# Performance work log

Measured on AMD Instinct MI355X. Metric: run time of the kernel, lower is better.

Reference implementation:

```python
import jax, jax.numpy as jnp
from jax import lax
import numpy as np

SLOPE = 0.1  # LeakyReLU negative slope used throughout DA_conv


def setup_inputs() -> dict:
    key = jax.random.key(0)
    ks = jax.random.split(key, 8)
    B, C, H, W = 16, 64, 160, 160
    Cout, red = 64, 8
    feat = jax.random.normal(ks[0], (B, C, H, W), dtype=jnp.float32)
    deg = jax.random.normal(ks[1], (B, C, 1, 1), dtype=jnp.float32)
    W1 = jax.random.normal(ks[2], (64, C), dtype=jnp.float32) * 0.05
    W2 = jax.random.normal(ks[3], (Cout * 9, 64), dtype=jnp.float32) * 0.05
    Wc = jax.random.normal(ks[4], (Cout, Cout), dtype=jnp.float32) * 0.05
    bc = jnp.zeros((Cout,), dtype=jnp.float32)
    Wd1 = jax.random.normal(ks[5], (red, C), dtype=jnp.float32) * 0.05
    Wd2 = jax.random.normal(ks[6], (Cout, red), dtype=jnp.float32) * 0.05
    return {"feat": feat, "deg": deg, "W1": W1, "W2": W2, "Wc": Wc,
            "bc": bc, "Wd1": Wd1, "Wd2": Wd2}


def reference(feat, deg, W1, W2, Wc, bc, Wd1, Wd2):
    B, C, H, W = feat.shape
    Cout = Wc.shape[0]
    KS = 3
    d = deg[:, :, 0, 0]  # [B, C]

    # --- dynamic per-sample, per-channel 3x3 kernel generation ---
    h = jax.nn.leaky_relu(d @ W1.T, SLOPE)            # [B, 64]
    k = (h @ W2.T).reshape(B * Cout, 1, KS, KS)        # [B*Cout, 1, 3, 3]

    # grouped depthwise conv: input [1, B*C, H, W], groups = B*C
    x = feat.reshape(1, B * C, H, W)
    out = lax.conv_general_dilated(
        x, k, window_strides=(1, 1), padding=[(1, 1), (1, 1)],
        dimension_numbers=("NCHW", "OIHW", "NCHW"),
        feature_group_count=B * C)
    out = jax.nn.leaky_relu(out, SLOPE).reshape(B, Cout, H, W)

    # 1x1 conv with bias (common.default_conv)
    out = jnp.einsum("oi,bihw->bohw", Wc, out) + bc[None, :, None, None]

    # --- channel attention branch (1x1 convs == matmuls on [B,C]) ---
    a = jax.nn.leaky_relu(jnp.einsum("ri,bi->br", Wd1, d), SLOPE)   # [B, red]
    att = jax.nn.sigmoid(jnp.einsum("or,br->bo", Wd2, a))           # [B, Cout]

    return out + feat * att[:, :, None, None]
```

## Files before the change

kernel.cpp:

```cpp
#include <hip/hip_runtime.h>
#include <hip/hip_bf16.h>
#include <math.h>

#define SLOPE 0.1f
#define B_ 16
#define C_ 64
#define H_ 160
#define W_ 160
#define HW_ (H_*W_)

typedef short bf16x8 __attribute__((ext_vector_type(8)));
typedef float f32x4  __attribute__((ext_vector_type(4)));
typedef unsigned int uint2v __attribute__((ext_vector_type(2)));

__device__ __forceinline__ float lrelu(float x) { return fmaxf(x, SLOPE * x); }
__device__ __forceinline__ unsigned f2bf(float x) {
  union { float f; unsigned u; } c; c.f = x;
  return (c.u + 0x7fffu + ((c.u >> 16) & 1u)) >> 16;
}
__device__ __forceinline__ float bf2f(unsigned short u) {
  union { unsigned u; float f; } c; c.u = ((unsigned)u) << 16; return c.f;
}

__device__ __forceinline__ void gl2lds16(const void* g, void* l) {
  __builtin_amdgcn_global_load_lds(
      (const __attribute__((address_space(1))) void*)g,
      (__attribute__((address_space(3))) void*)l, 16, 0, 0);
}

__global__ __launch_bounds__(64) void prep_kernel(
    const float* __restrict__ deg,
    const float* __restrict__ W1,
    const float* __restrict__ W2,
    const float* __restrict__ Wd1,
    const float* __restrict__ Wd2,
    float* __restrict__ ws) {
  const int b = blockIdx.x;
  const int j = threadIdx.x;
  __shared__ float sd[64], sh[64], sa[8];
  sd[j] = deg[b * 64 + j];
  __syncthreads();

  float acc = 0.f;
  for (int i = 0; i < 64; ++i) acc = fmaf(sd[i], W1[j * 64 + i], acc);
  sh[j] = lrelu(acc);

  if (j < 8) {
    float s = 0.f;
    for (int i = 0; i < 64; ++i) s = fmaf(sd[i], Wd1[j * 64 + i], s);
    sa[j] = lrelu(s);
  }
  __syncthreads();

  float kv[9];
#pragma unroll
  for (int t = 0; t < 9; ++t) kv[t] = 0.f;
  for (int l = 0; l < 64; ++l) {
    float hl = sh[l];
#pragma unroll
    for (int t = 0; t < 9; ++t) kv[t] = fmaf(hl, W2[(j * 9 + t) * 64 + l], kv[t]);
  }
  const int slot = ((j & 15) >> 2) * 16 + (j >> 4) * 4 + (j & 3);
  unsigned short* kw = (unsigned short*)(ws + 1024) + (b * 64 + slot) * 16;
#pragma unroll
  for (int t = 0; t < 9; ++t) kw[t] = (unsigned short)f2bf(kv[t]);
#pragma unroll
  for (int t = 9; t < 16; ++t) kw[t] = 0;

  float s2 = 0.f;
#pragma unroll
  for (int r = 0; r < 8; ++r) s2 = fmaf(Wd2[j * 8 + r], sa[r], s2);
  ws[b * 64 + j] = 1.f / (1.f + __expf(-s2));
}

__global__ __launch_bounds__(256, 4) void main_kernel(
    const float* __restrict__ feat,
    const float* __restrict__ Wc,
    const float* __restrict__ bc,
    const float* __restrict__ ws,
    float* __restrict__ out) {
  __shared__ __align__(16) float S[2][16][240];
  __shared__ __align__(16) unsigned short Tt[2048];
  __shared__ __align__(16) unsigned short Ff[2048];
  __shared__ __align__(16) unsigned short Kl[1024];

  const int rb  = blockIdx.x;
  const int bid = (rb & 7) * 400 + (rb >> 3);
  const int b   = bid / 200;
  const int rem = bid - b * 200;
  const int ty  = rem / 10, tx = rem - ty * 10;
  const int x0 = tx * 16, y0 = ty * 8;
  const int tid = threadIdx.x;
  const int lane = tid & 63, wid = tid >> 6;

  const float* __restrict__ attp  = ws + b * 64;
  const char*  __restrict__ kb8   = (const char*)(ws + 1024) + b * 2048;
  const float* __restrict__ plane = feat + (size_t)(b * 64) * HW_;

  const int ci = tid >> 4;
  const int q  = (tid >> 2) & 3;
  const int h  = tid & 3;
  const int nl = lane & 15, kg = lane >> 4;
  const int ochunk = wid * 16;

  const int srow = lane / 6;
  const int schk = lane - srow * 6;
  const int grow = min(max(y0 + srow - 1, 0), H_ - 1);
  const int gcol = min(max(x0 - 4 + schk * 4, 0), W_ - 4);
  const float* sp0 = plane + grow * W_ + gcol;

  union AF { bf16x8 v; unsigned short u[8]; };
  AF a[4];
  const unsigned short ab = (unsigned short)f2bf(attp[ochunk + nl]);
#pragma unroll
  for (int g = 0; g < 4; ++g) {
    const float4 w = *(const float4*)(Wc + (ochunk + nl) * 64 + g * 16 + 4 * kg);
    a[g].u[0] = (unsigned short)f2bf(w.x); a[g].u[1] = (unsigned short)f2bf(w.y);
    a[g].u[2] = (unsigned short)f2bf(w.z); a[g].u[3] = (unsigned short)f2bf(w.w);
#pragma unroll
    for (int j = 0; j < 4; ++j)
      a[g].u[4 + j] = (wid == g && nl == 4 * kg + j) ? ab : (unsigned short)0;
  }
  const float4 bcv = *(const float4*)(bc + ochunk + 4 * kg);

  asm volatile("s_waitcnt vmcnt(0)" ::: "memory");

  if (lane < 32) gl2lds16(kb8 + wid * 512 + lane * 16, &Kl[wid * 256]);
#define STAGE(g_, bf_) \
  if (lane < 60) { \
    const float* s_ = sp0 + (size_t)((g_) * 16 + wid * 4) * HW_; \
    gl2lds16(s_,            &S[bf_][wid * 4 + 0][0]); \
    gl2lds16(s_ + HW_,      &S[bf_][wid * 4 + 1][0]); \
    gl2lds16(s_ + 2 * HW_,  &S[bf_][wid * 4 + 2][0]); \
    gl2lds16(s_ + 3 * HW_,  &S[bf_][wid * 4 + 3][0]); \
  }
  STAGE(0, 0);
  STAGE(1, 1);

  f32x4 acc[8];
#pragma unroll
  for (int nt = 0; nt < 8; ++nt) acc[nt] = (f32x4){0.f, 0.f, 0.f, 0.f};

  const float mlz = (x0 == 0 && q == 0) ? 0.f : 1.f;
  const float mrz = (x0 == W_ - 16 && q == 3) ? 0.f : 1.f;

  const unsigned t_base = (unsigned)(uintptr_t)&Tt[0] + (unsigned)(lane * 8);
  const unsigned f_base = (unsigned)(uintptr_t)&Ff[0] + (unsigned)(lane * 8);
  union BU { bf16x8 v; uint2v qv[2]; };

#pragma unroll
  for (int g = 0; g < 4; ++g) {
    const int sb = g & 1;
    if (g < 3) {
      asm volatile("s_waitcnt vmcnt(4)" ::: "memory");
    } else {
      asm volatile("s_waitcnt vmcnt(0)" ::: "memory");
    }
    __builtin_amdgcn_sched_barrier(0);

    const unsigned short* kr = &Kl[(wid * 16 + g * 4 + (lane >> 4)) * 16];
    union KU { uint4 v; unsigned short u[8]; } k07;
    k07.v = *(const uint4*)kr;
    const unsigned short k8u = kr[8];
    float kk[9];
#pragma unroll
    for (int t = 0; t < 8; ++t) kk[t] = bf2f(k07.u[t]);
    kk[8] = bf2f(k8u);

    float rv[4][9];
#pragma unroll
    for (int rr = 0; rr < 4; ++rr) {
      const float* sp = &S[sb][ci][(2 * h + rr) * 24 + 4 * q];
      const f32x4 v0 = *(const f32x4*)sp;
      const f32x4 v1 = *(const f32x4*)(sp + 4);
      rv[rr][0] = v0[0]; rv[rr][1] = v0[1]; rv[rr][2] = v0[2];
      rv[rr][3] = v0[3] * mlz;
      rv[rr][4] = v1[0]; rv[rr][5] = v1[1]; rv[rr][6] = v1[2]; rv[rr][7] = v1[3];
      rv[rr][8] = sp[8] * mrz;
    }

#pragma unroll
    for (int rr = 0; rr < 2; ++rr) {
      const int srw = 2 * h + rr;
      const float mt = (srw == 0 && y0 == 0) ? 0.f : 1.f;
      const float mb = (srw == 7 && y0 == H_ - 8) ? 0.f : 1.f;
      float sv[4], fv[4];
#pragma unroll
      for (int j = 0; j < 4; ++j) {
        float ts = fmaf(rv[rr][j + 5], kk[2], fmaf(rv[rr][j + 4], kk[1], rv[rr][j + 3] * kk[0]));
        float cs = fmaf(rv[rr + 1][j + 5], kk[5], fmaf(rv[rr + 1][j + 4], kk[4], rv[rr + 1][j + 3] * kk[3]));
        float bs = fmaf(rv[rr + 2][j + 5], kk[8], fmaf(rv[rr + 2][j + 4], kk[7], rv[rr + 2][j + 3] * kk[6]));
        sv[j] = fmaf(mt, ts, fmaf(mb, bs, cs));
        fv[j] = rv[rr + 1][j + 4];
      }
      uint2v tq, fq;
      tq.x = f2bf(lrelu(sv[0])) | (f2bf(lrelu(sv[1])) << 16);
      tq.y = f2bf(lrelu(sv[2])) | (f2bf(lrelu(sv[3])) << 16);
      fq.x = f2bf(fv[0]) | (f2bf(fv[1]) << 16);
      fq.y = f2bf(fv[2]) | (f2bf(fv[3]) << 16);
      const int tidx = srw * 256 + ci * 16 + 4 * q;
      *(uint2v*)&Tt[tidx] = tq;
      *(uint2v*)&Ff[tidx] = fq;
    }

    if (g < 2) { STAGE(g + 2, sb); }

    asm volatile("s_waitcnt lgkmcnt(0)" ::: "memory");
    __builtin_amdgcn_sched_barrier(0);
    __builtin_amdgcn_s_barrier();
    __builtin_amdgcn_sched_barrier(0);

    if (wid == g) {
      uint2v t0, t1, t2, t3, t4, t5, t6, t7;
      uint2v f0, f1, f2, f3, f4, f5, f6, f7;
      asm volatile("ds_read_b64_tr_b16 %0, %1 offset:0"    : "=v"(t0) : "v"(t_base));
      asm volatile("ds_read_b64_tr_b16 %0, %1 offset:512"  : "=v"(t1) : "v"(t_base));
      asm volatile("ds_read_b64_tr_b16 %0, %1 offset:0"    : "=v"(f0) : "v"(f_base));
      asm volatile("ds_read_b64_tr_b16 %0, %1 offset:512"  : "=v"(f1) : "v"(f_base));
      asm volatile("ds_read_b64_tr_b16 %0, %1 offset:1024" : "=v"(t2) : "v"(t_base));
      asm volatile("ds_read_b64_tr_b16 %0, %1 offset:1536" : "=v"(t3) : "v"(t_base));
      asm volatile("ds_read_b64_tr_b16 %0, %1 offset:1024" : "=v"(f2) : "v"(f_base));
      asm volatile("ds_read_b64_tr_b16 %0, %1 offset:1536" : "=v"(f3) : "v"(f_base));
      asm volatile("s_waitcnt lgkmcnt(4)" ::: "memory");
      __builtin_amdgcn_sched_barrier(0);
      {
        BU u0, u1;
        u0.qv[0] = t0; u0.qv[1] = f0;
        u1.qv[0] = t1; u1.qv[1] = f1;
        acc[0] = __builtin_amdgcn_mfma_f32_16x16x32_bf16(a[g].v, u0.v, acc[0], 0, 0, 0);
        acc[1] = __builtin_amdgcn_mfma_f32_16x16x32_bf16(a[g].v, u1.v, acc[1], 0, 0, 0);
      }
      asm volatile("ds_read_b64_tr_b16 %0, %1 offset:2048" : "=v"(t4) : "v"(t_base));
      asm volatile("ds_read_b64_tr_b16 %0, %1 offset:2560" : "=v"(t5) : "v"(t_base));
      asm volatile("ds_read_b64_tr_b16 %0, %1 offset:2048" : "=v"(f4) : "v"(f_base));
      asm volatile("ds_read_b64_tr_b16 %0, %1 offset:2560" : "=v"(f5) : "v"(f_base));
      asm volatile("s_waitcnt lgkmcnt(4)" ::: "memory");
      __builtin_amdgcn_sched_barrier(0);
      {
        BU u2, u3;
        u2.qv[0] = t2; u2.qv[1] = f2;
        u3.qv[0] = t3; u3.qv[1] = f3;
        acc[2] = __builtin_amdgcn_mfma_f32_16x16x32_bf16(a[g].v, u2.v, acc[2], 0, 0, 0);
        acc[3] = __builtin_amdgcn_mfma_f32_16x16x32_bf16(a[g].v, u3.v, acc[3], 0, 0, 0);
      }
      asm volatile("ds_read_b64_tr_b16 %0, %1 offset:3072" : "=v"(t6) : "v"(t_base));
      asm volatile("ds_read_b64_tr_b16 %0, %1 offset:3584" : "=v"(t7) : "v"(t_base));
      asm volatile("ds_read_b64_tr_b16 %0, %1 offset:3072" : "=v"(f6) : "v"(f_base));
      asm volatile("ds_read_b64_tr_b16 %0, %1 offset:3584" : "=v"(f7) : "v"(f_base));
      asm volatile("s_waitcnt lgkmcnt(4)" ::: "memory");
      __builtin_amdgcn_sched_barrier(0);
      {
        BU u4, u5;
        u4.qv[0] = t4; u4.qv[1] = f4;
        u5.qv[0] = t5; u5.qv[1] = f5;
        acc[4] = __builtin_amdgcn_mfma_f32_16x16x32_bf16(a[g].v, u4.v, acc[4], 0, 0, 0);
        acc[5] = __builtin_amdgcn_mfma_f32_16x16x32_bf16(a[g].v, u5.v, acc[5], 0, 0, 0);
      }
      asm volatile("s_waitcnt lgkmcnt(0)" ::: "memory");
      __builtin_amdgcn_sched_barrier(0);
      {
        BU u6, u7;
        u6.qv[0] = t6; u6.qv[1] = f6;
        u7.qv[0] = t7; u7.qv[1] = f7;
        acc[6] = __builtin_amdgcn_mfma_f32_16x16x32_bf16(a[g].v, u6.v, acc[6], 0, 0, 0);
        acc[7] = __builtin_amdgcn_mfma_f32_16x16x32_bf16(a[g].v, u7.v, acc[7], 0, 0, 0);
      }
    } else {
      uint2v ta0, ta1, ta2, ta3, tb0, tb1, tb2, tb3;
      asm volatile("ds_read_b64_tr_b16 %0, %1 offset:0"    : "=v"(ta0) : "v"(t_base));
      asm volatile("ds_read_b64_tr_b16 %0, %1 offset:512"  : "=v"(ta1) : "v"(t_base));
      asm volatile("ds_read_b64_tr_b16 %0, %1 offset:1024" : "=v"(ta2) : "v"(t_base));
      asm volatile("ds_read_b64_tr_b16 %0, %1 offset:1536" : "=v"(ta3) : "v"(t_base));
      asm volatile("s_waitcnt lgkmcnt(0)" ::: "memory");
      __builtin_amdgcn_sched_barrier(0);
      asm volatile("ds_read_b64_tr_b16 %0, %1 offset:2048" : "=v"(tb0) : "v"(t_base));
      asm volatile("ds_read_b64_tr_b16 %0, %1 offset:2560" : "=v"(tb1) : "v"(t_base));
      asm volatile("ds_read_b64_tr_b16 %0, %1 offset:3072" : "=v"(tb2) : "v"(t_base));
      asm volatile("ds_read_b64_tr_b16 %0, %1 offset:3584" : "=v"(tb3) : "v"(t_base));
      {
        BU u0, u1, u2, u3;
        u0.qv[0] = ta0; u0.qv[1] = (uint2v){0u, 0u};
        u1.qv[0] = ta1; u1.qv[1] = (uint2v){0u, 0u};
        u2.qv[0] = ta2; u2.qv[1] = (uint2v){0u, 0u};
        u3.qv[0] = ta3; u3.qv[1] = (uint2v){0u, 0u};
        acc[0] = __builtin_amdgcn_mfma_f32_16x16x32_bf16(a[g].v, u0.v, acc[0], 0, 0, 0);
        acc[1] = __builtin_amdgcn_mfma_f32_16x16x32_bf16(a[g].v, u1.v, acc[1], 0, 0, 0);
        acc[2] = __builtin_amdgcn_mfma_f32_16x16x32_bf16(a[g].v, u2.v, acc[2], 0, 0, 0);
        acc[3] = __builtin_amdgcn_mfma_f32_16x16x32_bf16(a[g].v, u3.v, acc[3], 0, 0, 0);
      }
      asm volatile("s_waitcnt lgkmcnt(0)" ::: "memory");
      __builtin_amdgcn_sched_barrier(0);
      {
        BU u4, u5, u6, u7;
        u4.qv[0] = tb0; u4.qv[1] = (uint2v){0u, 0u};
        u5.qv[0] = tb1; u5.qv[1] = (uint2v){0u, 0u};
        u6.qv[0] = tb2; u6.qv[1] = (uint2v){0u, 0u};
        u7.qv[0] = tb3; u7.qv[1] = (uint2v){0u, 0u};
        acc[4] = __builtin_amdgcn_mfma_f32_16x16x32_bf16(a[g].v, u4.v, acc[4], 0, 0, 0);
        acc[5] = __builtin_amdgcn_mfma_f32_16x16x32_bf16(a[g].v, u5.v, acc[5], 0, 0, 0);
        acc[6] = __builtin_amdgcn_mfma_f32_16x16x32_bf16(a[g].v, u6.v, acc[6], 0, 0, 0);
        acc[7] = __builtin_amdgcn_mfma_f32_16x16x32_bf16(a[g].v, u7.v, acc[7], 0, 0, 0);
      }
    }
    __builtin_amdgcn_s_barrier();
    __builtin_amdgcn_sched_barrier(0);
  }
#undef STAGE

  const int ob = ochunk + 4 * kg;
  float* __restrict__ outb = out + (size_t)(b * 64) * HW_;
#pragma unroll
  for (int nt = 0; nt < 8; ++nt) {
    const int off = (y0 + nt) * W_ + x0 + nl;
    outb[(size_t)(ob + 0) * HW_ + off] = acc[nt][0] + bcv.x;
    outb[(size_t)(ob + 1) * HW_ + off] = acc[nt][1] + bcv.y;
    outb[(size_t)(ob + 2) * HW_ + off] = acc[nt][2] + bcv.z;
    outb[(size_t)(ob + 3) * HW_ + off] = acc[nt][3] + bcv.w;
  }
}

extern "C" void kernel_launch(void* const* d_in, const int* in_sizes, int n_in,
                              void* d_out, int out_size, void* d_ws, size_t ws_size,
                              hipStream_t stream) {
  const float* feat = (const float*)d_in[0];
  const float* deg  = (const float*)d_in[1];
  const float* W1   = (const float*)d_in[2];
  const float* W2   = (const float*)d_in[3];
  const float* Wc   = (const float*)d_in[4];
  const float* bc   = (const float*)d_in[5];
  const float* Wd1  = (const float*)d_in[6];
  const float* Wd2  = (const float*)d_in[7];
  float* out = (float*)d_out;
  float* ws  = (float*)d_ws;

  prep_kernel<<<dim3(B_), dim3(64), 0, stream>>>(deg, W1, W2, Wd1, Wd2, ws);
  main_kernel<<<dim3(3200), dim3(256), 0, stream>>>(feat, Wc, bc, ws, out);
}
```

Before: 67.17 us.

## Convert main kernel to persistent blocks with atomic tile scheduler

The main kernel launches 1024 persistent blocks that grab 8x16 tiles from a global atomic counter, which prep_kernel resets, instead of launching one block per tile. Per-block setup such as the bf16 Wc fragments and bias is hoisted out of the tile loop. The per-sample kernel weights are packed at 12 halves per channel instead of 16, and the attention diagonal fragment is rebuilt per tile. The aim is to cut block launch and setup overhead and balance load, at the cost of an atomic and a __syncthreads per tile and no cross-tile overlap of loads.

```diff
diff --git a/kernel.cpp b/kernel.cpp
--- a/kernel.cpp
+++ b/kernel.cpp
@@ -8,6 +8,8 @@
 #define H_ 160
 #define W_ 160
 #define HW_ (H_*W_)
+#define NTILES 3200
+#define WS_CTR_OFF 28672
 
 typedef short bf16x8 __attribute__((ext_vector_type(8)));
 typedef float f32x4  __attribute__((ext_vector_type(4)));
@@ -61,71 +63,59 @@
     for (int t = 0; t < 9; ++t) kv[t] = fmaf(hl, W2[(j * 9 + t) * 64 + l], kv[t]);
   }
   const int slot = ((j & 15) >> 2) * 16 + (j >> 4) * 4 + (j & 3);
-  unsigned short* kw = (unsigned short*)(ws + 1024) + (b * 64 + slot) * 16;
+  unsigned short* kw = (unsigned short*)((char*)ws + 4096) + (b * 64 + slot) * 12;
 #pragma unroll
   for (int t = 0; t < 9; ++t) kw[t] = (unsigned short)f2bf(kv[t]);
-#pragma unroll
-  for (int t = 9; t < 16; ++t) kw[t] = 0;
+  kw[9] = 0; kw[10] = 0; kw[11] = 0;
 
   float s2 = 0.f;
 #pragma unroll
   for (int r = 0; r < 8; ++r) s2 = fmaf(Wd2[j * 8 + r], sa[r], s2);
   ws[b * 64 + j] = 1.f / (1.f + __expf(-s2));
+
+  if (b == 0 && j == 0) *(unsigned*)((char*)ws + WS_CTR_OFF) = 0u;
 }
 
 __global__ __launch_bounds__(256, 4) void main_kernel(
     const float* __restrict__ feat,
     const float* __restrict__ Wc,
     const float* __restrict__ bc,
-    const float* __restrict__ ws,
+    float* __restrict__ ws,
     float* __restrict__ out) {
   __shared__ __align__(16) float S[2][16][240];
   __shared__ __align__(16) unsigned short Tt[2048];
   __shared__ __align__(16) unsigned short Ff[2048];
-  __shared__ __align__(16) unsigned short Kl[1024];
-
-  const int rb  = blockIdx.x;
-  const int bid = (rb & 7) * 400 + (rb >> 3);
-  const int b   = bid / 200;
-  const int rem = bid - b * 200;
-  const int ty  = rem / 10, tx = rem - ty * 10;
-  const int x0 = tx * 16, y0 = ty * 8;
+  __shared__ __align__(16) unsigned short Kl[768];
+  __shared__ int sTile;
+
   const int tid = threadIdx.x;
   const int lane = tid & 63, wid = tid >> 6;
-
-  const float* __restrict__ attp  = ws + b * 64;
-  const char*  __restrict__ kb8   = (const char*)(ws + 1024) + b * 2048;
-  const float* __restrict__ plane = feat + (size_t)(b * 64) * HW_;
-
   const int ci = tid >> 4;
   const int q  = (tid >> 2) & 3;
   const int h  = tid & 3;
   const int nl = lane & 15, kg = lane >> 4;
   const int ochunk = wid * 16;
-
   const int srow = lane / 6;
   const int schk = lane - srow * 6;
-  const int grow = min(max(y0 + srow - 1, 0), H_ - 1);
-  const int gcol = min(max(x0 - 4 + schk * 4, 0), W_ - 4);
-  const float* sp0 = plane + grow * W_ + gcol;
+
+  unsigned* ctr = (unsigned*)((char*)ws + WS_CTR_OFF);
 
   union AF { bf16x8 v; unsigned short u[8]; };
   AF a[4];
-  const unsigned short ab = (unsigned short)f2bf(attp[ochunk + nl]);
 #pragma unroll
   for (int g = 0; g < 4; ++g) {
     const float4 w = *(const float4*)(Wc + (ochunk + nl) * 64 + g * 16 + 4 * kg);
     a[g].u[0] = (unsigned short)f2bf(w.x); a[g].u[1] = (unsigned short)f2bf(w.y);
     a[g].u[2] = (unsigned short)f2bf(w.z); a[g].u[3] = (unsigned short)f2bf(w.w);
-#pragma unroll
-    for (int j = 0; j < 4; ++j)
-      a[g].u[4 + j] = (wid == g && nl == 4 * kg + j) ? ab : (unsigned short)0;
+    a[g].u[4] = 0; a[g].u[5] = 0; a[g].u[6] = 0; a[g].u[7] = 0;
   }
   const float4 bcv = *(const float4*)(bc + ochunk + 4 * kg);
-
   asm volatile("s_waitcnt vmcnt(0)" ::: "memory");
 
-  if (lane < 32) gl2lds16(kb8 + wid * 512 + lane * 16, &Kl[wid * 256]);
+  const unsigned t_base = (unsigned)(uintptr_t)&Tt[0] + (unsigned)(lane * 8);
+  const unsigned f_base = (unsigned)(uintptr_t)&Ff[0] + (unsigned)(lane * 8);
+  union BU { bf16x8 v; uint2v qv[2]; };
+
 #define STAGE(g_, bf_) \
   if (lane < 60) { \
     const float* s_ = sp0 + (size_t)((g_) * 16 + wid * 4) * HW_; \
@@ -134,189 +124,215 @@
     gl2lds16(s_ + 2 * HW_,  &S[bf_][wid * 4 + 2][0]); \
     gl2lds16(s_ + 3 * HW_,  &S[bf_][wid * 4 + 3][0]); \
   }
-  STAGE(0, 0);
-  STAGE(1, 1);
-
-  f32x4 acc[8];
-#pragma unroll
-  for (int nt = 0; nt < 8; ++nt) acc[nt] = (f32x4){0.f, 0.f, 0.f, 0.f};
-
-  const float mlz = (x0 == 0 && q == 0) ? 0.f : 1.f;
-  const float mrz = (x0 == W_ - 16 && q == 3) ? 0.f : 1.f;
-
-  const unsigned t_base = (unsigned)(uintptr_t)&Tt[0] + (unsigned)(lane * 8);
-  const unsigned f_base = (unsigned)(uintptr_t)&Ff[0] + (unsigned)(lane * 8);
-  union BU { bf16x8 v; uint2v qv[2]; };
-
-#pragma unroll
-  for (int g = 0; g < 4; ++g) {
-    const int sb = g & 1;
-    if (g < 3) {
-      asm volatile("s_waitcnt vmcnt(4)" ::: "memory");
-    } else {
-      asm volatile("s_waitcnt vmcnt(0)" ::: "memory");
-    }
-    __builtin_amdgcn_sched_barrier(0);
-
-    const unsigned short* kr = &Kl[(wid * 16 + g * 4 + (lane >> 4)) * 16];
-    union KU { uint4 v; unsigned short u[8]; } k07;
-    k07.v = *(const uint4*)kr;
-    const unsigned short k8u = kr[8];
-    float kk[9];
-#pragma unroll
-    for (int t = 0; t < 8; ++t) kk[t] = bf2f(k07.u[t]);
-    kk[8] = bf2f(k8u);
-
-    float rv[4][9];
-#pragma unroll
-    for (int rr = 0; rr < 4; ++rr) {
-      const float* sp = &S[sb][ci][(2 * h + rr) * 24 + 4 * q];
-      const f32x4 v0 = *(const f32x4*)sp;
-      const f32x4 v1 = *(const f32x4*)(sp + 4);
-      rv[rr][0] = v0[0]; rv[rr][1] = v0[1]; rv[rr][2] = v0[2];
-      rv[rr][3] = v0[3] * mlz;
-      rv[rr][4] = v1[0]; rv[rr][5] = v1[1]; rv[rr][6] = v1[2]; rv[rr][7] = v1[3];
-      rv[rr][8] = sp[8] * mrz;
-    }
-
-#pragma unroll
-    for (int rr = 0; rr < 2; ++rr) {
-      const int srw = 2 * h + rr;
-      const float mt = (srw == 0 && y0 == 0) ? 0.f : 1.f;
-      const float mb = (srw == 7 && y0 == H_ - 8) ? 0.f : 1.f;
-      float sv[4], fv[4];
-#pragma unroll
-      for (int j = 0; j < 4; ++j) {
-        float ts = fmaf(rv[rr][j + 5], kk[2], fmaf(rv[rr][j + 4], kk[1], rv[rr][j + 3] * kk[0]));
-        float cs = fmaf(rv[rr + 1][j + 5], kk[5], fmaf(rv[rr + 1][j + 4], kk[4], rv[rr + 1][j + 3] * kk[3]));
-        float bs = fmaf(rv[rr + 2][j + 5], kk[8], fmaf(rv[rr + 2][j + 4], kk[7], rv[rr + 2][j + 3] * kk[6]));
-        sv[j] = fmaf(mt, ts, fmaf(mb, bs, cs));
-        fv[j] = rv[rr + 1][j + 4];
+
+  for (;;) {
+    if (tid == 0) sTile = (int)atomicAdd(ctr, 1u);
+    __syncthreads();
+    const int tl = sTile;
+    if (tl >= NTILES) break;
+
+    const int b   = tl / 200;
+    const int rem = tl - b * 200;
+    const int ty  = rem / 10, tx = rem - ty * 10;
+    const int x0 = tx * 16, y0 = ty * 8;
+
+    const float* __restrict__ plane = feat + (size_t)(b * 64) * HW_;
+    const char*  __restrict__ kb8   = (const char*)ws + 4096 + b * 1536;
+    const float abf = ws[b * 64 + ochunk + nl];
+
+    const int grow = min(max(y0 + srow - 1, 0), H_ - 1);
+    const int gcol = min(max(x0 - 4 + schk * 4, 0), W_ - 4);
+    const float* sp0 = plane + grow * W_ + gcol;
+    const float mlz = (x0 == 0 && q == 0) ? 0.f : 1.f;
+    const float mrz = (x0 == W_ - 16 && q == 3) ? 0.f : 1.f;
+
+    if (lane < 24) gl2lds16(kb8 + wid * 384 + lane * 16, &Kl[wid * 192]);
+    STAGE(0, 0);
+    STAGE(1, 1);
+
+    f32x4 acc[8];
+#pragma unroll
+    for (int nt = 0; nt < 8; ++nt) acc[nt] = (f32x4){0.f, 0.f, 0.f, 0.f};
+
+#pragma unroll
+    for (int g = 0; g < 4; ++g) {
+      const int sb = g & 1;
+      if (g < 3) {
+        asm volatile("s_waitcnt vmcnt(4)" ::: "memory");
+      } else {
+        asm volatile("s_waitcnt vmcnt(0)" ::: "memory");
       }
-      uint2v tq, fq;
-      tq.x = f2bf(lrelu(sv[0])) | (f2bf(lrelu(sv[1])) << 16);
-      tq.y = f2bf(lrelu(sv[2])) | (f2bf(lrelu(sv[3])) << 16);
-      fq.x = f2bf(fv[0]) | (f2bf(fv[1]) << 16);
-      fq.y = f2bf(fv[2]) | (f2bf(fv[3]) << 16);
-      const int tidx = srw * 256 + ci * 16 + 4 * q;
-      *(uint2v*)&Tt[tidx] = tq;
-      *(uint2v*)&Ff[tidx] = fq;
-    }
-
-    if (g < 2) { STAGE(g + 2, sb); }
-
-    asm volatile("s_waitcnt lgkmcnt(0)" ::: "memory");
-    __builtin_amdgcn_sched_barrier(0);
-    __builtin_amdgcn_s_barrier();
-    __builtin_amdgcn_sched_barrier(0);
-
-    if (wid == g) {
-      uint2v t0, t1, t2, t3, t4, t5, t6, t7;
-      uint2v f0, f1, f2, f3, f4, f5, f6, f7;
-      asm volatile("ds_read_b64_tr_b16 %0, %1 offset:0"    : "=v"(t0) : "v"(t_base));
-      asm volatile("ds_read_b64_tr_b16 %0, %1 offset:512"  : "=v"(t1) : "v"(t_base));
-      asm volatile("ds_read_b64_tr_b16 %0, %1 offset:0"    : "=v"(f0) : "v"(f_base));
-      asm volatile("ds_read_b64_tr_b16 %0, %1 offset:512"  : "=v"(f1) : "v"(f_base));
-      asm volatile("ds_read_b64_tr_b16 %0, %1 offset:1024" : "=v"(t2) : "v"(t_base));
-      asm volatile("ds_read_b64_tr_b16 %0, %1 offset:1536" : "=v"(t3) : "v"(t_base));
-      asm volatile("ds_read_b64_tr_b16 %0, %1 offset:1024" : "=v"(f2) : "v"(f_base));
-      asm volatile("ds_read_b64_tr_b16 %0, %1 offset:1536" : "=v"(f3) : "v"(f_base));
-      asm volatile("s_waitcnt lgkmcnt(4)" ::: "memory");
       __builtin_amdgcn_sched_barrier(0);
-      {
-        BU u0, u1;
-        u0.qv[0] = t0; u0.qv[1] = f0;
-        u1.qv[0] = t1; u1.qv[1] = f1;
-        acc[0] = __builtin_amdgcn_mfma_f32_16x16x32_bf16(a[g].v, u0.v, acc[0], 0, 0, 0);
-        acc[1] = __builtin_amdgcn_mfma_f32_16x16x32_bf16(a[g].v, u1.v, acc[1], 0, 0, 0);
+
+      const unsigned short* kr = &Kl[(wid * 16 + g * 4 + (lane >> 4)) * 12];
+      union KU { uint2v v; unsigned short u[4]; };
+      KU kA, kB;
+      kA.v = *(const uint2v*)(kr);
+      kB.v = *(const uint2v*)(kr + 4);
+      const unsigned short k8u = kr[8];
+      float kk[9];
+#pragma unroll
+      for (int t = 0; t < 4; ++t) { kk[t] = bf2f(kA.u[t]); kk[4 + t] = bf2f(kB.u[t]); }
+      kk[8] = bf2f(k8u);
+
+      float rv[4][9];
+#pragma unroll
+      for (int rr = 0; rr < 4; ++rr) {
+        const float* sp = &S[sb][ci][(2 * h + rr) * 24 + 4 * q];
+        const f32x4 v0 = *(const f32x4*)sp;
+        const f32x4 v1 = *(const f32x4*)(sp + 4);
+        rv[rr][0] = v0[0]; rv[rr][1] = v0[1]; rv[rr][2] = v0[2];
+        rv[rr][3] = v0[3] * mlz;
+        rv[rr][4] = v1[0]; rv[rr][5] = v1[1]; rv[rr][6] = v1[2]; rv[rr][7] = v1[3];
+        rv[rr][8] = sp[8] * mrz;
       }
-      asm volatile("ds_read_b64_tr_b16 %0, %1 offset:2048" : "=v"(t4) : "v"(t_base));
-      asm volatile("ds_read_b64_tr_b16 %0, %1 offset:2560" : "=v"(t5) : "v"(t_base));
-      asm volatile("ds_read_b64_tr_b16 %0, %1 offset:2048" : "=v"(f4) : "v"(f_base));
-      asm volatile("ds_read_b64_tr_b16 %0, %1 offset:2560" : "=v"(f5) : "v"(f_base));
-      asm volatile("s_waitcnt lgkmcnt(4)" ::: "memory");
-      __builtin_amdgcn_sched_barrier(0);
-      {
-        BU u2, u3;
-        u2.qv[0] = t2; u2.qv[1] = f2;
-        u3.qv[0] = t3; u3.qv[1] = f3;
-        acc[2] = __builtin_amdgcn_mfma_f32_16x16x32_bf16(a[g].v, u2.v, acc[2], 0, 0, 0);
-        acc[3] = __builtin_amdgcn_mfma_f32_16x16x32_bf16(a[g].v, u3.v, acc[3], 0, 0, 0);
+
+#pragma unroll
+      for (int rr = 0; rr < 2; ++rr) {
+        const int srw = 2 * h + rr;
+        const float mt = (srw == 0 && y0 == 0) ? 0.f : 1.f;
+        const float mb = (srw == 7 && y0 == H_ - 8) ? 0.f : 1.f;
+        float sv[4], fv[4];
+#pragma unroll
+        for (int j = 0; j < 4; ++j) {
+          float ts = fmaf(rv[rr][j + 5], kk[2], fmaf(rv[rr][j + 4], kk[1], rv[rr][j + 3] * kk[0]));
+          float cs = fmaf(rv[rr + 1][j + 5], kk[5], fmaf(rv[rr + 1][j + 4], kk[4], rv[rr + 1][j + 3] * kk[3]));
+          float bs = fmaf(rv[rr + 2][j + 5], kk[8], fmaf(rv[rr + 2][j + 4], kk[7], rv[rr + 2][j + 3] * kk[6]));
+          sv[j] = fmaf(mt, ts, fmaf(mb, bs, cs));
+          fv[j] = rv[rr + 1][j + 4];
+        }
+        uint2v tq, fq;
+        tq.x = f2bf(lrelu(sv[0])) | (f2bf(lrelu(sv[1])) << 16);
+        tq.y = f2bf(lrelu(sv[2])) | (f2bf(lrelu(sv[3])) << 16);
+        fq.x = f2bf(fv[0]) | (f2bf(fv[1]) << 16);
+        fq.y = f2bf(fv[2]) | (f2bf(fv[3]) << 16);
+        const int tidx = srw * 256 + ci * 16 + 4 * q;
+        *(uint2v*)&Tt[tidx] = tq;
+        *(uint2v*)&Ff[tidx] = fq;
       }
-      asm volatile("ds_read_b64_tr_b16 %0, %1 offset:3072" : "=v"(t6) : "v"(t_base));
-      asm volatile("ds_read_b64_tr_b16 %0, %1 offset:3584" : "=v"(t7) : "v"(t_base));
-      asm volatile("ds_read_b64_tr_b16 %0, %1 offset:3072" : "=v"(f6) : "v"(f_base));
-      asm volatile("ds_read_b64_tr_b16 %0, %1 offset:3584" : "=v"(f7) : "v"(f_base));
-      asm volatile("s_waitcnt lgkmcnt(4)" ::: "memory");
-      __builtin_amdgcn_sched_barrier(0);
-      {
-        BU u4, u5;
-        u4.qv[0] = t4; u4.qv[1] = f4;
-        u5.qv[0] = t5; u5.qv[1] = f5;
-        acc[4] = __builtin_amdgcn_mfma_f32_16x16x32_bf16(a[g].v, u4.v, acc[4], 0, 0, 0);
-        acc[5] = __builtin_amdgcn_mfma_f32_16x16x32_bf16(a[g].v, u5.v, acc[5], 0, 0, 0);
-      }
+
+      if (g < 2) { STAGE(g + 2, sb); }
+
       asm volatile("s_waitcnt lgkmcnt(0)" ::: "memory");
       __builtin_amdgcn_sched_barrier(0);
-      {
-        BU u6, u7;
-        u6.qv[0] = t6; u6.qv[1] = f6;
-        u7.qv[0] = t7; u7.qv[1] = f7;
-        acc[6] = __builtin_amdgcn_mfma_f32_16x16x32_bf16(a[g].v, u6.v, acc[6], 0, 0, 0);
-        acc[7] = __builtin_amdgcn_mfma_f32_16x16x32_bf16(a[g].v, u7.v, acc[7], 0, 0, 0);
+      __builtin_amdgcn_s_barrier();
+      __builtin_amdgcn_sched_barrier(0);
+
+      if (wid == g) {
+        AF adiag;
+        adiag.v = a[g].v;
+        const unsigned short abu = (unsigned short)f2bf(abf);
+#pragma unroll
+        for (int j = 0; j < 4; ++j)
+          adiag.u[4 + j] = (nl == 4 * kg + j) ? abu : (unsigned short)0;
+
+        uint2v t0, t1, t2, t3, t4, t5, t6, t7;
+        uint2v f0, f1, f2, f3, f4, f5, f6, f7;
+        asm volatile("ds_read_b64_tr_b16 %0, %1 offset:0"    : "=v"(t0) : "v"(t_base));
+        asm volatile("ds_read_b64_tr_b16 %0, %1 offset:512"  : "=v"(t1) : "v"(t_base));
+        asm volatile("ds_read_b64_tr_b16 %0, %1 offset:0"    : "=v"(f0) : "v"(f_base));
+        asm volatile("ds_read_b64_tr_b16 %0, %1 offset:512"  : "=v"(f1) : "v"(f_base));
+        asm volatile("ds_read_b64_tr_b16 %0, %1 offset:1024" : "=v"(t2) : "v"(t_base));
+        asm volatile("ds_read_b64_tr_b16 %0, %1 offset:1536" : "=v"(t3) : "v"(t_base));
+        asm volatile("ds_read_b64_tr_b16 %0, %1 offset:1024" : "=v"(f2) : "v"(f_base));
+        asm volatile("ds_read_b64_tr_b16 %0, %1 offset:1536" : "=v"(f3) : "v"(f_base));
+        asm volatile("s_waitcnt lgkmcnt(4)" ::: "memory");
+        __builtin_amdgcn_sched_barrier(0);
+        {
+          BU u0, u1;
+          u0.qv[0] = t0; u0.qv[1] = f0;
+          u1.qv[0] = t1; u1.qv[1] = f1;
+          acc[0] = __builtin_amdgcn_mfma_f32_16x16x32_bf16(adiag.v, u0.v, acc[0], 0, 0, 0);
+          acc[1] = __builtin_amdgcn_mfma_f32_16x16x32_bf16(adiag.v, u1.v, acc[1], 0, 0, 0);
+        }
+        asm volatile("ds_read_b64_tr_b16 %0, %1 offset:2048" : "=v"(t4) : "v"(t_base));
+        asm volatile("ds_read_b64_tr_b16 %0, %1 offset:2560" : "=v"(t5) : "v"(t_base));
+        asm volatile("ds_read_b64_tr_b16 %0, %1 offset:2048" : "=v"(f4) : "v"(f_base));
+        asm volatile("ds_read_b64_tr_b16 %0, %1 offset:2560" : "=v"(f5) : "v"(f_base));
+        asm volatile("s_waitcnt lgkmcnt(4)" ::: "memory");
+        __builtin_amdgcn_sched_barrier(0);
+        {
+          BU u2, u3;
+          u2.qv[0] = t2; u2.qv[1] = f2;
+          u3.qv[0] = t3; u3.qv[1] = f3;
+          acc[2] = __builtin_amdgcn_mfma_f32_16x16x32_bf16(adiag.v, u2.v, acc[2], 0, 0, 0);
+          acc[3] = __builtin_amdgcn_mfma_f32_16x16x32_bf16(adiag.v, u3.v, acc[3], 0, 0, 0);
+        }
+        asm volatile("ds_read_b64_tr_b16 %0, %1 offset:3072" : "=v"(t6) : "v"(t_base));
+        asm volatile("ds_read_b64_tr_b16 %0, %1 offset:3584" : "=v"(t7) : "v"(t_base));
+        asm volatile("ds_read_b64_tr_b16 %0, %1 offset:3072" : "=v"(f6) : "v"(f_base));
+        asm volatile("ds_read_b64_tr_b16 %0, %1 offset:3584" : "=v"(f7) : "v"(f_base));
+        asm volatile("s_waitcnt lgkmcnt(4)" ::: "memory");
+        __builtin_amdgcn_sched_barrier(0);
+        {
+          BU u4, u5;
+          u4.qv[0] = t4; u4.qv[1] = f4;
+          u5.qv[0] = t5; u5.qv[1] = f5;
+          acc[4] = __builtin_amdgcn_mfma_f32_16x16x32_bf16(adiag.v, u4.v, acc[4], 0, 0, 0);
+          acc[5] = __builtin_amdgcn_mfma_f32_16x16x32_bf16(adiag.v, u5.v, acc[5], 0, 0, 0);
+        }
+        asm volatile("s_waitcnt lgkmcnt(0)" ::: "memory");
+        __builtin_amdgcn_sched_barrier(0);
+        {
+          BU u6, u7;
+          u6.qv[0] = t6; u6.qv[1] = f6;
+          u7.qv[0] = t7; u7.qv[1] = f7;
+          acc[6] = __builtin_amdgcn_mfma_f32_16x16x32_bf16(adiag.v, u6.v, acc[6], 0, 0, 0);
+          acc[7] = __builtin_amdgcn_mfma_f32_16x16x32_bf16(adiag.v, u7.v, acc[7], 0, 0, 0);
+        }
+      } else {
+        uint2v ta0, ta1, ta2, ta3, tb0, tb1, tb2, tb3;
+        asm volatile("ds_read_b64_tr_b16 %0, %1 offset:0"    : "=v"(ta0) : "v"(t_base));
+        asm volatile("ds_read_b64_tr_b16 %0, %1 offset:512"  : "=v"(ta1) : "v"(t_base));
+        asm volatile("ds_read_b64_tr_b16 %0, %1 offset:1024" : "=v"(ta2) : "v"(t_base));
+        asm volatile("ds_read_b64_tr_b16 %0, %1 offset:1536" : "=v"(ta3) : "v"(t_base));
+        asm volatile("s_waitcnt lgkmcnt(0)" ::: "memory");
+        __builtin_amdgcn_sched_barrier(0);
+        asm volatile("ds_read_b64_tr_b16 %0, %1 offset:2048" : "=v"(tb0) : "v"(t_base));
+        asm volatile("ds_read_b64_tr_b16 %0, %1 offset:2560" : "=v"(tb1) : "v"(t_base));
+        asm volatile("ds_read_b64_tr_b16 %0, %1 offset:3072" : "=v"(tb2) : "v"(t_base));
+        asm volatile("ds_read_b64_tr_b16 %0, %1 offset:3584" : "=v"(tb3) : "v"(t_base));
+        {
+          BU u0, u1, u2, u3;
+          u0.qv[0] = ta0; u0.qv[1] = (uint2v){0u, 0u};
+          u1.qv[0] = ta1; u1.qv[1] = (uint2v){0u, 0u};
+          u2.qv[0] = ta2; u2.qv[1] = (uint2v){0u, 0u};
+          u3.qv[0] = ta3; u3.qv[1] = (uint2v){0u, 0u};
+          acc[0] = __builtin_amdgcn_mfma_f32_16x16x32_bf16(a[g].v, u0.v, acc[0], 0, 0, 0);
+          acc[1] = __builtin_amdgcn_mfma_f32_16x16x32_bf16(a[g].v, u1.v, acc[1], 0, 0, 0);
+          acc[2] = __builtin_amdgcn_mfma_f32_16x16x32_bf16(a[g].v, u2.v, acc[2], 0, 0, 0);
+          acc[3] = __builtin_amdgcn_mfma_f32_16x16x32_bf16(a[g].v, u3.v, acc[3], 0, 0, 0);
+        }
+        asm volatile("s_waitcnt lgkmcnt(0)" ::: "memory");
+        __builtin_amdgcn_sched_barrier(0);
+        {
+          BU u4, u5, u6, u7;
+          u4.qv[0] = tb0; u4.qv[1] = (uint2v){0u, 0u};
+          u5.qv[0] = tb1; u5.qv[1] = (uint2v){0u, 0u};
+          u6.qv[0] = tb2; u6.qv[1] = (uint2v){0u, 0u};
+          u7.qv[0] = tb3; u7.qv[1] = (uint2v){0u, 0u};
+          acc[4] = __builtin_amdgcn_mfma_f32_16x16x32_bf16(a[g].v, u4.v, acc[4], 0, 0, 0);
+          acc[5] = __builtin_amdgcn_mfma_f32_16x16x32_bf16(a[g].v, u5.v, acc[5], 0, 0, 0);
+          acc[6] = __builtin_amdgcn_mfma_f32_16x16x32_bf16(a[g].v, u6.v, acc[6], 0, 0, 0);
+          acc[7] = __builtin_amdgcn_mfma_f32_16x16x32_bf16(a[g].v, u7.v, acc[7], 0, 0, 0);
+        }
       }
-    } else {
-      uint2v ta0, ta1, ta2, ta3, tb0, tb1, tb2, tb3;
-      asm volatile("ds_read_b64_tr_b16 %0, %1 offset:0"    : "=v"(ta0) : "v"(t_base));
-      asm volatile("ds_read_b64_tr_b16 %0, %1 offset:512"  : "=v"(ta1) : "v"(t_base));
-      asm volatile("ds_read_b64_tr_b16 %0, %1 offset:1024" : "=v"(ta2) : "v"(t_base));
-      asm volatile("ds_read_b64_tr_b16 %0, %1 offset:1536" : "=v"(ta3) : "v"(t_base));
-      asm volatile("s_waitcnt lgkmcnt(0)" ::: "memory");
+      __builtin_amdgcn_s_barrier();
       __builtin_amdgcn_sched_barrier(0);
-      asm volatile("ds_read_b64_tr_b16 %0, %1 offset:2048" : "=v"(tb0) : "v"(t_base));
-      asm volatile("ds_read_b64_tr_b16 %0, %1 offset:2560" : "=v"(tb1) : "v"(t_base));
-      asm volatile("ds_read_b64_tr_b16 %0, %1 offset:3072" : "=v"(tb2) : "v"(t_base));
-      asm volatile("ds_read_b64_tr_b16 %0, %1 offset:3584" : "=v"(tb3) : "v"(t_base));
-      {
-        BU u0, u1, u2, u3;
-        u0.qv[0] = ta0; u0.qv[1] = (uint2v){0u, 0u};
-        u1.qv[0] = ta1; u1.qv[1] = (uint2v){0u, 0u};
-        u2.qv[0] = ta2; u2.qv[1] = (uint2v){0u, 0u};
-        u3.qv[0] = ta3; u3.qv[1] = (uint2v){0u, 0u};
-        acc[0] = __builtin_amdgcn_mfma_f32_16x16x32_bf16(a[g].v, u0.v, acc[0], 0, 0, 0);
-        acc[1] = __builtin_amdgcn_mfma_f32_16x16x32_bf16(a[g].v, u1.v, acc[1], 0, 0, 0);
-        acc[2] = __builtin_amdgcn_mfma_f32_16x16x32_bf16(a[g].v, u2.v, acc[2], 0, 0, 0);
-        acc[3] = __builtin_amdgcn_mfma_f32_16x16x32_bf16(a[g].v, u3.v, acc[3], 0, 0, 0);
-      }
-      asm volatile("s_waitcnt lgkmcnt(0)" ::: "memory");
-      __builtin_amdgcn_sched_barrier(0);
-      {
-        BU u4, u5, u6, u7;
-        u4.qv[0] = tb0; u4.qv[1] = (uint2v){0u, 0u};
-        u5.qv[0] = tb1; u5.qv[1] = (uint2v){0u, 0u};
-        u6.qv[0] = tb2; u6.qv[1] = (uint2v){0u, 0u};
-        u7.qv[0] = tb3; u7.qv[1] = (uint2v){0u, 0u};
-        acc[4] = __builtin_amdgcn_mfma_f32_16x16x32_bf16(a[g].v, u4.v, acc[4], 0, 0, 0);
-        acc[5] = __builtin_amdgcn_mfma_f32_16x16x32_bf16(a[g].v, u5.v, acc[5], 0, 0, 0);
-        acc[6] = __builtin_amdgcn_mfma_f32_16x16x32_bf16(a[g].v, u6.v, acc[6], 0, 0, 0);
-        acc[7] = __builtin_amdgcn_mfma_f32_16x16x32_bf16(a[g].v, u7.v, acc[7], 0, 0, 0);
-      }
     }
-    __builtin_amdgcn_s_barrier();
-    __builtin_amdgcn_sched_barrier(0);
+
+    const int ob = ochunk + 4 * kg;
+    float* __restrict__ outb = out + (size_t)(b * 64) * HW_;
+#pragma unroll
+    for (int nt = 0; nt < 8; ++nt) {
+      const int off = (y0 + nt) * W_ + x0 + nl;
+      outb[(size_t)(ob + 0) * HW_ + off] = acc[nt][0] + bcv.x;
+      outb[(size_t)(ob + 1) * HW_ + off] = acc[nt][1] + bcv.y;
+      outb[(size_t)(ob + 2) * HW_ + off] = acc[nt][2] + bcv.z;
+      outb[(size_t)(ob + 3) * HW_ + off] = acc[nt][3] + bcv.w;
+    }
   }
 #undef STAGE
-
-  const int ob = ochunk + 4 * kg;
-  float* __restrict__ outb = out + (size_t)(b * 64) * HW_;
-#pragma unroll
-  for (int nt = 0; nt < 8; ++nt) {
-    const int off = (y0 + nt) * W_ + x0 + nl;
-    outb[(size_t)(ob + 0) * HW_ + off] = acc[nt][0] + bcv.x;
-    outb[(size_t)(ob + 1) * HW_ + off] = acc[nt][1] + bcv.y;
-    outb[(size_t)(ob + 2) * HW_ + off] = acc[nt][2] + bcv.z;
-    outb[(size_t)(ob + 3) * HW_ + off] = acc[nt][3] + bcv.w;
-  }
 }
 
 extern "C" void kernel_launch(void* const* d_in, const int* in_sizes, int n_in,
@@ -334,5 +350,5 @@
   float* ws  = (float*)d_ws;
 
   prep_kernel<<<dim3(B_), dim3(64), 0, stream>>>(deg, W1, W2, Wd1, Wd2, ws);
-  main_kernel<<<dim3(3200), dim3(256), 0, stream>>>(feat, Wc, bc, ws, out);
-}
+  main_kernel<<<dim3(1024), dim3(256), 0, stream>>>(feat, Wc, bc, ws, out);
+}
```

After: 105.4 us. 1.57x slower.
